# Optimization experiments

Hardware: AMD Instinct MI355X
Metric: run time of the kernel (lower is better)

Reference implementation:

```python
import jax, jax.numpy as jnp
import numpy as np

N, E = 50000, 800000
DIN, DH, DOUT = 128, 128, 64


def setup_inputs() -> dict:
    key = jax.random.key(0)
    k = jax.random.split(key, 6)
    node_features = jax.random.normal(k[0], (N, DIN), dtype=jnp.float32)
    edge_src = jax.random.randint(k[1], (E,), 0, N)
    edge_dst = jax.random.randint(k[2], (E,), 0, N)
    # Glorot-ish init for the two GCNConv weight matrices, zero bias (PyG default bias=True)
    W1 = jax.random.normal(k[3], (DIN, DH), dtype=jnp.float32) * (1.0 / np.sqrt(DIN))
    b1 = jnp.zeros((DH,), dtype=jnp.float32)
    W2 = jax.random.normal(k[4], (DH, DOUT), dtype=jnp.float32) * (1.0 / np.sqrt(DH))
    b2 = jnp.zeros((DOUT,), dtype=jnp.float32)
    return {"node_features": node_features, "edge_src": edge_src, "edge_dst": edge_dst,
            "W1": W1, "b1": b1, "W2": W2, "b2": b2}


def gcn_conv(x, W, b, src, dst, n):
    """PyG GCNConv: add self-loops, symmetric D^-1/2 (A+I) D^-1/2 normalization."""
    xw = x @ W  # [n, d_out]
    loops = jnp.arange(n, dtype=src.dtype)
    s = jnp.concatenate([src, loops])  # edges + self-loops
    d = jnp.concatenate([dst, loops])
    deg = jax.ops.segment_sum(jnp.ones_like(d, dtype=xw.dtype), d, num_segments=n)
    dinv = jnp.where(deg > 0, jax.lax.rsqrt(deg), 0.0)
    norm = dinv[s] * dinv[d]  # [E + n]
    msg = xw[s] * norm[:, None]  # gather + scale (memory-bound)
    out = jax.ops.segment_sum(msg, d, num_segments=n)  # scatter-add
    return out + b


def reference(node_features, edge_src, edge_dst, W1, b1, W2, b2):
    n = node_features.shape[0]
    h = gcn_conv(node_features, W1, b1, edge_src, edge_dst, n)
    h = jax.nn.relu(h)  # dropout omitted (inference / eval mode)
    h = gcn_conv(h, W2, b2, edge_src, edge_dst, n)
    # EdgePredictor: per-edge dot product of endpoint representations
    score = jnp.sum(h[edge_src] * h[edge_dst], axis=-1)  # [E]
    return score
```

## Files before the change

### kernel.cpp

```cpp
#include <hip/hip_runtime.h>
#include <hip/hip_bf16.h>
#include <type_traits>


#define DIN 128
#define DH  128
#define DOUT 64
#define BSH 7
#define BNODES 128
#define CAP 2560
#define QSH 13
#define POISON 0xAAAAAAAAu

typedef __attribute__((ext_vector_type(8))) short short8;
typedef __attribute__((ext_vector_type(4))) float floatx4;

__device__ inline float2 bf2_to_f2(unsigned u) {
    union { unsigned i; float f; } a, b;
    a.i = u << 16;
    b.i = u & 0xffff0000u;
    return make_float2(a.f, b.f);
}
__device__ inline float bf_to_f(unsigned short u) {
    union { unsigned i; float f; } a;
    a.i = ((unsigned)u) << 16;
    return a.f;
}
__device__ inline unsigned short f_to_bf(float f) {
    union { float f; unsigned i; } v; v.f = f;
    unsigned r = v.i + 0x7fffu + ((v.i >> 16) & 1u);
    return (unsigned short)(r >> 16);
}

__global__ __launch_bounds__(256) void place_gemm1_kernel(
    const int* __restrict__ src, const int* __restrict__ dst,
    unsigned* __restrict__ cursor, uint2* __restrict__ tmp, int E, int EB,
    const float* __restrict__ X, const float* __restrict__ W1,
    unsigned short* __restrict__ Y, int nrows) {
    __shared__ __align__(16) char smem[69632];
    int bid = blockIdx.x, t = threadIdx.x;

    if (bid < EB) {
        int* hist = (int*)smem;
        int* cur  = hist + 512;
        hist[t] = 0; hist[t + 256] = 0;
        __syncthreads();
        int base = bid * 4096 + t;
        int d[16];
#pragma unroll
        for (int it = 0; it < 16; ++it) {
            int e = base + it * 256;
            d[it] = (e < E) ? dst[e] : -1;
            if (d[it] >= 0) atomicAdd(&hist[d[it] >> BSH], 1);
        }
        __syncthreads();
#pragma unroll
        for (int k = t; k < 512; k += 256)
            if (hist[k])
                cur[k] = (int)(atomicAdd(&cursor[k], (unsigned)hist[k]) - POISON);
        __syncthreads();
#pragma unroll
        for (int it = 0; it < 16; ++it) {
            int e = base + it * 256;
            if (d[it] >= 0) {
                int bkt = d[it] >> BSH;
                int r = atomicAdd(&cur[bkt], 1);
                if (r >= 0 && r < CAP)
                    tmp[(size_t)bkt * CAP + r] =
                        make_uint2((unsigned)src[e] |
                                   ((unsigned)(d[it] & (BNODES - 1)) << 16),
                                   (unsigned)e);
            }
        }
        return;
    }

    constexpr int KP = 136;
    unsigned short* Xs = (unsigned short*)smem;
    unsigned short* Wt = Xs + 128 * KP;
    int row0 = (bid - EB) * 128;

#pragma unroll
    for (int it = 0; it < 16; ++it) {
        int idx = it * 256 + t;
        int r = idx >> 5;
        int c4 = (idx & 31) * 4;
        int gr = row0 + r; if (gr >= nrows) gr = nrows - 1;
        float4 v = *(const float4*)(X + (size_t)gr * 128 + c4);
        ushort4 p;
        p.x = f_to_bf(v.x); p.y = f_to_bf(v.y);
        p.z = f_to_bf(v.z); p.w = f_to_bf(v.w);
        *(ushort4*)&Xs[r * KP + c4] = p;
    }
#pragma unroll
    for (int it = 0; it < 16; ++it) {
        int idx = it * 256 + t;
        int n = idx >> 5;
        int k4 = (idx & 31) * 4;
        ushort4 p;
        p.x = f_to_bf(W1[(size_t)(k4 + 0) * 128 + n]);
        p.y = f_to_bf(W1[(size_t)(k4 + 1) * 128 + n]);
        p.z = f_to_bf(W1[(size_t)(k4 + 2) * 128 + n]);
        p.w = f_to_bf(W1[(size_t)(k4 + 3) * 128 + n]);
        *(ushort4*)&Wt[n * KP + k4] = p;
    }
    __syncthreads();

    int wv = t >> 6, lane = t & 63;
    int lr = lane & 15;
    int lk = (lane >> 4) * 8;
    int rw = wv * 32;

    floatx4 acc[2][8];
#pragma unroll
    for (int rt = 0; rt < 2; ++rt)
#pragma unroll
        for (int ct = 0; ct < 8; ++ct) acc[rt][ct] = (floatx4){0.f, 0.f, 0.f, 0.f};

#pragma unroll
    for (int kk = 0; kk < 128; kk += 32) {
        short8 a[2], b[8];
#pragma unroll
        for (int rt = 0; rt < 2; ++rt)
            a[rt] = *(const short8*)&Xs[(rw + rt * 16 + lr) * KP + kk + lk];
#pragma unroll
        for (int ct = 0; ct < 8; ++ct)
            b[ct] = *(const short8*)&Wt[(ct * 16 + lr) * KP + kk + lk];
#pragma unroll
        for (int rt = 0; rt < 2; ++rt)
#pragma unroll
            for (int ct = 0; ct < 8; ++ct)
                acc[rt][ct] = __builtin_amdgcn_mfma_f32_16x16x32_bf16(
                    a[rt], b[ct], acc[rt][ct], 0, 0, 0);
    }
#pragma unroll
    for (int rt = 0; rt < 2; ++rt) {
#pragma unroll
        for (int i = 0; i < 4; ++i) {
            int grow = row0 + rw + rt * 16 + (lane >> 4) * 4 + i;
            if (grow >= nrows) continue;
#pragma unroll
            for (int ct = 0; ct < 8; ++ct)
                Y[(size_t)grow * 128 + ct * 16 + lr] = f_to_bf(acc[rt][ct][i]);
        }
    }
}

__global__ __launch_bounds__(512) void bucket_csr_kernel(const uint2* __restrict__ tmp,
                                                         const unsigned* __restrict__ cursor,
                                                         int* __restrict__ row_beg,
                                                         int* __restrict__ row_end,
                                                         float* __restrict__ dinv,
                                                         int* __restrict__ col,
                                                         int* __restrict__ eidx, int N) {
    __shared__ int hist[1024], cur[1024];
    __shared__ int wsum[8];
    __shared__ unsigned ebuf[CAP];
    __shared__ unsigned ibuf[CAP];
    __shared__ unsigned ssrc[CAP];
    __shared__ unsigned sidx[CAP];
    int b = blockIdx.x, t = threadIdx.x;
    int lane = t & 63, wv = t >> 6;
    int size = (int)(cursor[b] - POISON);
    if (size < 0) size = 0;
    if (size > CAP) size = CAP;
    size_t rbase = (size_t)b * CAP;
    hist[t] = 0; hist[t + 512] = 0;
    __syncthreads();
    for (int i = t; i < size; i += 512) {
        uint2 e = tmp[rbase + i];
        ebuf[i] = e.x;
        ibuf[i] = e.y;
        int key = (int)(e.x >> 16) * 8 + (int)((e.x & 0xffffu) >> QSH);
        atomicAdd(&hist[key], 1);
    }
    __syncthreads();
    int l0 = hist[t * 2], l1 = hist[t * 2 + 1];
    int s = l0 + l1;
    int run = s;
#pragma unroll
    for (int off = 1; off < 64; off <<= 1) {
        int u = __shfl_up(run, off);
        if (lane >= off) run += u;
    }
    if (lane == 63) wsum[wv] = run;
    __syncthreads();
    int woff = 0;
#pragma unroll
    for (int k = 0; k < 8; ++k) woff += (k < wv) ? wsum[k] : 0;
    int excl = woff + run - s;
    hist[t * 2] = excl;       cur[t * 2] = excl;
    hist[t * 2 + 1] = excl + l0; cur[t * 2 + 1] = excl + l0;
    __syncthreads();
    if (t < BNODES) {
        int node = b * BNODES + t;
        if (node < N) {
            int nbeg = hist[t * 8];
            int nend = (t == BNODES - 1) ? size : hist[t * 8 + 8];
            row_beg[node] = (int)rbase + nbeg;
            row_end[node] = (int)rbase + nend;
            dinv[node] = rsqrtf((float)(nend - nbeg + 1));
        }
    }
    __syncthreads();
    for (int i = t; i < size; i += 512) {
        unsigned e = ebuf[i];
        int key = (int)(e >> 16) * 8 + (int)((e & 0xffffu) >> QSH);
        int r = atomicAdd(&cur[key], 1);
        ssrc[r] = e & 0xffffu;
        sidx[r] = ibuf[i];
    }
    __syncthreads();
    for (int i = t; i < size; i += 512) {
        col[rbase + i]  = (int)ssrc[i];
        eidx[rbase + i] = (int)sidx[i];
    }
}

__global__ __launch_bounds__(256) void agg1_kernel(const unsigned short* __restrict__ y1,
                                                   const int* __restrict__ row_beg,
                                                   const int* __restrict__ row_end,
                                                   const int* __restrict__ col,
                                                   const float* __restrict__ dinv,
                                                   const float* __restrict__ b1,
                                                   unsigned short* __restrict__ h1, int n) {
    int w = (blockIdx.x * 256 + threadIdx.x) >> 6;
    int lane = threadIdx.x & 63;
    if (w >= n) return;
    float dw = dinv[w];
    float acc0, acc1;
    {
        float2 t2 = bf2_to_f2(*(const unsigned*)(y1 + (size_t)w * 128 + lane * 2));
        acc0 = dw * t2.x; acc1 = dw * t2.y;
    }
    int beg = row_beg[w], end = row_end[w];
    int i = beg;
    for (; i + 8 <= end; i += 8) {
        int s[8];
#pragma unroll
        for (int u = 0; u < 8; ++u) s[u] = col[i + u];
        float dv[8];
#pragma unroll
        for (int u = 0; u < 8; ++u) dv[u] = dinv[s[u]];
        unsigned tv[8];
#pragma unroll
        for (int u = 0; u < 8; ++u)
            tv[u] = *(const unsigned*)(y1 + (size_t)s[u] * 128 + lane * 2);
#pragma unroll
        for (int u = 0; u < 8; ++u) {
            float2 f = bf2_to_f2(tv[u]);
            acc0 = fmaf(dv[u], f.x, acc0);
            acc1 = fmaf(dv[u], f.y, acc1);
        }
    }
    for (; i < end; ++i) {
        int s = col[i];
        float dv = dinv[s];
        float2 f = bf2_to_f2(*(const unsigned*)(y1 + (size_t)s * 128 + lane * 2));
        acc0 = fmaf(dv, f.x, acc0);
        acc1 = fmaf(dv, f.y, acc1);
    }
    float r0 = fmaxf(fmaf(dw, acc0, b1[lane * 2]), 0.f);
    float r1 = fmaxf(fmaf(dw, acc1, b1[lane * 2 + 1]), 0.f);
    unsigned pk = (unsigned)f_to_bf(r0) | ((unsigned)f_to_bf(r1) << 16);
    *(unsigned*)(h1 + (size_t)w * 128 + lane * 2) = pk;
}

__global__ __launch_bounds__(256) void mfma_gemm2_kernel(const unsigned short* __restrict__ X,
                                                         const float* __restrict__ W,
                                                         const float* __restrict__ dinv,
                                                         unsigned short* __restrict__ Y,
                                                         int nrows) {
    constexpr int KP = 136;
    __shared__ unsigned short Xs[128 * KP];
    __shared__ unsigned short Wt[64 * KP];
    int tid = threadIdx.x;
    int row0 = blockIdx.x * 128;

#pragma unroll
    for (int it = 0; it < 8; ++it) {
        int idx = it * 256 + tid;
        int r = idx >> 4;
        int c8 = (idx & 15) * 8;
        int gr = row0 + r; if (gr >= nrows) gr = nrows - 1;
        uint4 v = *(const uint4*)(X + (size_t)gr * 128 + c8);
        *(uint4*)&Xs[r * KP + c8] = v;
    }
#pragma unroll
    for (int it = 0; it < 8; ++it) {
        int idx = it * 256 + tid;
        int n = idx >> 5;
        int k4 = (idx & 31) * 4;
        ushort4 p;
        p.x = f_to_bf(W[(size_t)(k4 + 0) * 64 + n]);
        p.y = f_to_bf(W[(size_t)(k4 + 1) * 64 + n]);
        p.z = f_to_bf(W[(size_t)(k4 + 2) * 64 + n]);
        p.w = f_to_bf(W[(size_t)(k4 + 3) * 64 + n]);
        *(ushort4*)&Wt[n * KP + k4] = p;
    }
    __syncthreads();

    int wv = tid >> 6, lane = tid & 63;
    int lr = lane & 15;
    int lk = (lane >> 4) * 8;
    int rw = wv * 32;

    floatx4 acc[2][4];
#pragma unroll
    for (int rt = 0; rt < 2; ++rt)
#pragma unroll
        for (int ct = 0; ct < 4; ++ct) acc[rt][ct] = (floatx4){0.f, 0.f, 0.f, 0.f};

#pragma unroll
    for (int kk = 0; kk < 128; kk += 32) {
        short8 a[2], b[4];
#pragma unroll
        for (int rt = 0; rt < 2; ++rt)
            a[rt] = *(const short8*)&Xs[(rw + rt * 16 + lr) * KP + kk + lk];
#pragma unroll
        for (int ct = 0; ct < 4; ++ct)
            b[ct] = *(const short8*)&Wt[(ct * 16 + lr) * KP + kk + lk];
#pragma unroll
        for (int rt = 0; rt < 2; ++rt)
#pragma unroll
            for (int ct = 0; ct < 4; ++ct)
                acc[rt][ct] = __builtin_amdgcn_mfma_f32_16x16x32_bf16(
                    a[rt], b[ct], acc[rt][ct], 0, 0, 0);
    }
#pragma unroll
    for (int rt = 0; rt < 2; ++rt) {
#pragma unroll
        for (int i = 0; i < 4; ++i) {
            int grow = row0 + rw + rt * 16 + (lane >> 4) * 4 + i;
            if (grow >= nrows) continue;
            float dv = dinv[grow];
#pragma unroll
            for (int ct = 0; ct < 4; ++ct)
                Y[(size_t)grow * 64 + ct * 16 + lr] = f_to_bf(acc[rt][ct][i] * dv);
        }
    }
}

__global__ __launch_bounds__(256) void agg2_kernel(const unsigned short* __restrict__ y,
                                                   const int* __restrict__ row_beg,
                                                   const int* __restrict__ row_end,
                                                   const int* __restrict__ col,
                                                   const float* __restrict__ dinv,
                                                   const float* __restrict__ bias,
                                                   unsigned short* __restrict__ out, int n) {
    int w = (blockIdx.x * 256 + threadIdx.x) >> 6;
    int lane = threadIdx.x & 63;
    if (w >= n) return;
    float acc = bf_to_f(y[(size_t)w * 64 + lane]);
    int beg = row_beg[w], end = row_end[w];
    int i = beg;
    for (; i + 8 <= end; i += 8) {
        int s[8];
#pragma unroll
        for (int u = 0; u < 8; ++u) s[u] = col[i + u];
        unsigned short tv[8];
#pragma unroll
        for (int u = 0; u < 8; ++u) tv[u] = y[(size_t)s[u] * 64 + lane];
#pragma unroll
        for (int u = 0; u < 8; ++u) acc += bf_to_f(tv[u]);
    }
    for (; i < end; ++i) acc += bf_to_f(y[(size_t)col[i] * 64 + lane]);
    float r = fmaf(dinv[w], acc, bias[lane]);
    out[(size_t)w * 64 + lane] = f_to_bf(r);
}

__global__ __launch_bounds__(256) void score_csr_kernel(const unsigned short* __restrict__ h2,
                                                        const int* __restrict__ row_beg,
                                                        const int* __restrict__ row_end,
                                                        const int* __restrict__ col,
                                                        const int* __restrict__ eidx,
                                                        float* __restrict__ out, int n) {
    int w = (blockIdx.x * 256 + threadIdx.x) >> 6;
    int lane = threadIdx.x & 63;
    if (w >= n) return;
    int q = lane & 7;
    uint4 hd = *(const uint4*)(h2 + (size_t)w * 64 + q * 8);
    float d0[8];
    { float2 f;
      f = bf2_to_f2(hd.x); d0[0] = f.x; d0[1] = f.y;
      f = bf2_to_f2(hd.y); d0[2] = f.x; d0[3] = f.y;
      f = bf2_to_f2(hd.z); d0[4] = f.x; d0[5] = f.y;
      f = bf2_to_f2(hd.w); d0[6] = f.x; d0[7] = f.y; }
    int beg = row_beg[w], end = row_end[w];
    int g = lane >> 3;
    for (int i = beg; i < end; i += 8) {
        int ei = i + g;
        bool ok = ei < end;
        int s = ok ? col[ei] : 0;
        uint4 hs = *(const uint4*)(h2 + (size_t)s * 64 + q * 8);
        float v = 0.f;
        float2 f;
        f = bf2_to_f2(hs.x); v = fmaf(d0[0], f.x, v); v = fmaf(d0[1], f.y, v);
        f = bf2_to_f2(hs.y); v = fmaf(d0[2], f.x, v); v = fmaf(d0[3], f.y, v);
        f = bf2_to_f2(hs.z); v = fmaf(d0[4], f.x, v); v = fmaf(d0[5], f.y, v);
        f = bf2_to_f2(hs.w); v = fmaf(d0[6], f.x, v); v = fmaf(d0[7], f.y, v);
        v += __shfl_xor(v, 4);
        v += __shfl_xor(v, 2);
        v += __shfl_xor(v, 1);
        if (ok && q == 0) out[eidx[ei]] = v;
    }
}

extern "C" void kernel_launch(void* const* d_in, const int* in_sizes, int n_in,
                              void* d_out, int out_size, void* d_ws, size_t ws_size,
                              hipStream_t stream) {
    const float* X   = (const float*)d_in[0];
    const int*   src = (const int*)d_in[1];
    const int*   dst = (const int*)d_in[2];
    const float* W1  = (const float*)d_in[3];
    const float* b1  = (const float*)d_in[4];
    const float* W2  = (const float*)d_in[5];
    const float* b2  = (const float*)d_in[6];
    float* score = (float*)d_out;

    const int N = in_sizes[0] / DIN;
    const int E = in_sizes[1];
    const int nbuck = (N + BNODES - 1) / BNODES;
    const int EB = (E + 4095) / 4096;
    const int GB = (N + 127) / 128;

    auto align = [](size_t x) { return (x + 255) & ~(size_t)255; };
    char* p = (char*)d_ws;
    unsigned* cursor = (unsigned*)p;        p += align(512 * 4);
    int*   row_beg = (int*)p;               p += align((size_t)N * 4);
    int*   row_end = (int*)p;               p += align((size_t)N * 4);
    float* dinv    = (float*)p;             p += align((size_t)N * 4);
    int*   col     = (int*)p;               p += align((size_t)nbuck * CAP * 4);
    int*   eidx    = (int*)p;               p += align((size_t)nbuck * CAP * 4);
    uint2* tmp     = (uint2*)p;             p += align((size_t)nbuck * CAP * 8);
    unsigned short* y1 = (unsigned short*)p; p += align((size_t)N * DH * 2);
    unsigned short* h1 = (unsigned short*)p; p += align((size_t)N * DH * 2);
    unsigned short* y2 = y1;
    unsigned short* h2 = y1 + (size_t)N * DOUT;

    place_gemm1_kernel<<<EB + GB, 256, 0, stream>>>(src, dst, cursor, tmp, E, EB,
                                                    X, W1, y1, N);
    bucket_csr_kernel<<<nbuck, 512, 0, stream>>>(tmp, cursor, row_beg, row_end,
                                                 dinv, col, eidx, N);

    int agg_blocks = (N + 3) / 4;
    agg1_kernel<<<agg_blocks, 256, 0, stream>>>(y1, row_beg, row_end, col,
                                                dinv, b1, h1, N);

    mfma_gemm2_kernel<<<GB, 256, 0, stream>>>(h1, W2, dinv, y2, N);

    agg2_kernel<<<agg_blocks, 256, 0, stream>>>(y2, row_beg, row_end, col,
                                                dinv, b2, h2, N);
    score_csr_kernel<<<agg_blocks, 256, 0, stream>>>(h2, row_beg, row_end,
                                                     col, eidx, score, N);
}
```

Before: 232.0 us.

## Widen gather loads in aggregation kernels and unroll score loop over two edges

Both aggregation kernels now split each wavefront into four 16-lane groups. Each group gathers a different neighbor row with 16-byte (agg1) or 8-byte (agg2) vector loads, so one load instruction covers four edges instead of one. Partial sums are combined across groups with xor shuffles, and only the first group writes the output. The score kernel processes two edge batches per iteration for more loads in flight, and all three kernels get an occupancy hint in launch bounds. In exchange there is extra shuffle work, more registers per thread, and some wasted lanes on tail iterations for low-degree nodes.

```diff
diff --git a/kernel.cpp b/kernel.cpp
--- a/kernel.cpp
+++ b/kernel.cpp
@@ -217,53 +217,84 @@
     }
 }
 
-__global__ __launch_bounds__(256) void agg1_kernel(const unsigned short* __restrict__ y1,
-                                                   const int* __restrict__ row_beg,
-                                                   const int* __restrict__ row_end,
-                                                   const int* __restrict__ col,
-                                                   const float* __restrict__ dinv,
-                                                   const float* __restrict__ b1,
-                                                   unsigned short* __restrict__ h1, int n) {
+__global__ __launch_bounds__(256, 8) void agg1_kernel(const unsigned short* __restrict__ y1,
+                                                      const int* __restrict__ row_beg,
+                                                      const int* __restrict__ row_end,
+                                                      const int* __restrict__ col,
+                                                      const float* __restrict__ dinv,
+                                                      const float* __restrict__ b1,
+                                                      unsigned short* __restrict__ h1, int n) {
     int w = (blockIdx.x * 256 + threadIdx.x) >> 6;
     int lane = threadIdx.x & 63;
     if (w >= n) return;
+    int q = lane & 15;
+    int g = lane >> 4;
     float dw = dinv[w];
-    float acc0, acc1;
+    float acc[8];
     {
-        float2 t2 = bf2_to_f2(*(const unsigned*)(y1 + (size_t)w * 128 + lane * 2));
-        acc0 = dw * t2.x; acc1 = dw * t2.y;
+        uint4 hv = *(const uint4*)(y1 + (size_t)w * 128 + q * 8);
+        float selfw = (g == 0) ? dw : 0.f;
+        float2 f;
+        f = bf2_to_f2(hv.x); acc[0] = selfw * f.x; acc[1] = selfw * f.y;
+        f = bf2_to_f2(hv.y); acc[2] = selfw * f.x; acc[3] = selfw * f.y;
+        f = bf2_to_f2(hv.z); acc[4] = selfw * f.x; acc[5] = selfw * f.y;
+        f = bf2_to_f2(hv.w); acc[6] = selfw * f.x; acc[7] = selfw * f.y;
     }
     int beg = row_beg[w], end = row_end[w];
     int i = beg;
-    for (; i + 8 <= end; i += 8) {
-        int s[8];
-#pragma unroll
-        for (int u = 0; u < 8; ++u) s[u] = col[i + u];
-        float dv[8];
-#pragma unroll
-        for (int u = 0; u < 8; ++u) dv[u] = dinv[s[u]];
-        unsigned tv[8];
-#pragma unroll
-        for (int u = 0; u < 8; ++u)
-            tv[u] = *(const unsigned*)(y1 + (size_t)s[u] * 128 + lane * 2);
-#pragma unroll
-        for (int u = 0; u < 8; ++u) {
-            float2 f = bf2_to_f2(tv[u]);
-            acc0 = fmaf(dv[u], f.x, acc0);
-            acc1 = fmaf(dv[u], f.y, acc1);
-        }
-    }
-    for (; i < end; ++i) {
-        int s = col[i];
-        float dv = dinv[s];
-        float2 f = bf2_to_f2(*(const unsigned*)(y1 + (size_t)s * 128 + lane * 2));
-        acc0 = fmaf(dv, f.x, acc0);
-        acc1 = fmaf(dv, f.y, acc1);
-    }
-    float r0 = fmaxf(fmaf(dw, acc0, b1[lane * 2]), 0.f);
-    float r1 = fmaxf(fmaf(dw, acc1, b1[lane * 2 + 1]), 0.f);
-    unsigned pk = (unsigned)f_to_bf(r0) | ((unsigned)f_to_bf(r1) << 16);
-    *(unsigned*)(h1 + (size_t)w * 128 + lane * 2) = pk;
+    for (; i + 16 <= end; i += 16) {
+        int s4[4];
+#pragma unroll
+        for (int u = 0; u < 4; ++u) s4[u] = col[i + u * 4 + g];
+        float dv[4];
+#pragma unroll
+        for (int u = 0; u < 4; ++u) dv[u] = dinv[s4[u]];
+        uint4 tv[4];
+#pragma unroll
+        for (int u = 0; u < 4; ++u)
+            tv[u] = *(const uint4*)(y1 + (size_t)s4[u] * 128 + q * 8);
+#pragma unroll
+        for (int u = 0; u < 4; ++u) {
+            float2 f;
+            f = bf2_to_f2(tv[u].x); acc[0] = fmaf(dv[u], f.x, acc[0]); acc[1] = fmaf(dv[u], f.y, acc[1]);
+            f = bf2_to_f2(tv[u].y); acc[2] = fmaf(dv[u], f.x, acc[2]); acc[3] = fmaf(dv[u], f.y, acc[3]);
+            f = bf2_to_f2(tv[u].z); acc[4] = fmaf(dv[u], f.x, acc[4]); acc[5] = fmaf(dv[u], f.y, acc[5]);
+            f = bf2_to_f2(tv[u].w); acc[6] = fmaf(dv[u], f.x, acc[6]); acc[7] = fmaf(dv[u], f.y, acc[7]);
+        }
+    }
+    for (; i < end; i += 4) {
+        int r = i + g;
+        bool ok = r < end;
+        int sv = ok ? col[r] : col[i];
+        float dv = ok ? dinv[sv] : 0.f;
+        uint4 tv = *(const uint4*)(y1 + (size_t)sv * 128 + q * 8);
+        float2 f;
+        f = bf2_to_f2(tv.x); acc[0] = fmaf(dv, f.x, acc[0]); acc[1] = fmaf(dv, f.y, acc[1]);
+        f = bf2_to_f2(tv.y); acc[2] = fmaf(dv, f.x, acc[2]); acc[3] = fmaf(dv, f.y, acc[3]);
+        f = bf2_to_f2(tv.z); acc[4] = fmaf(dv, f.x, acc[4]); acc[5] = fmaf(dv, f.y, acc[5]);
+        f = bf2_to_f2(tv.w); acc[6] = fmaf(dv, f.x, acc[6]); acc[7] = fmaf(dv, f.y, acc[7]);
+    }
+#pragma unroll
+    for (int j = 0; j < 8; ++j) {
+        acc[j] += __shfl_xor(acc[j], 16);
+        acc[j] += __shfl_xor(acc[j], 32);
+    }
+    if (g == 0) {
+        float r0 = fmaxf(fmaf(dw, acc[0], b1[q * 8 + 0]), 0.f);
+        float r1 = fmaxf(fmaf(dw, acc[1], b1[q * 8 + 1]), 0.f);
+        float r2 = fmaxf(fmaf(dw, acc[2], b1[q * 8 + 2]), 0.f);
+        float r3 = fmaxf(fmaf(dw, acc[3], b1[q * 8 + 3]), 0.f);
+        float r4 = fmaxf(fmaf(dw, acc[4], b1[q * 8 + 4]), 0.f);
+        float r5 = fmaxf(fmaf(dw, acc[5], b1[q * 8 + 5]), 0.f);
+        float r6 = fmaxf(fmaf(dw, acc[6], b1[q * 8 + 6]), 0.f);
+        float r7 = fmaxf(fmaf(dw, acc[7], b1[q * 8 + 7]), 0.f);
+        uint4 pk;
+        pk.x = (unsigned)f_to_bf(r0) | ((unsigned)f_to_bf(r1) << 16);
+        pk.y = (unsigned)f_to_bf(r2) | ((unsigned)f_to_bf(r3) << 16);
+        pk.z = (unsigned)f_to_bf(r4) | ((unsigned)f_to_bf(r5) << 16);
+        pk.w = (unsigned)f_to_bf(r6) | ((unsigned)f_to_bf(r7) << 16);
+        *(uint4*)(h1 + (size_t)w * 128 + q * 8) = pk;
+    }
 }
 
 __global__ __launch_bounds__(256) void mfma_gemm2_kernel(const unsigned short* __restrict__ X,
@@ -341,40 +372,77 @@
     }
 }
 
-__global__ __launch_bounds__(256) void agg2_kernel(const unsigned short* __restrict__ y,
-                                                   const int* __restrict__ row_beg,
-                                                   const int* __restrict__ row_end,
-                                                   const int* __restrict__ col,
-                                                   const float* __restrict__ dinv,
-                                                   const float* __restrict__ bias,
-                                                   unsigned short* __restrict__ out, int n) {
+__global__ __launch_bounds__(256, 8) void agg2_kernel(const unsigned short* __restrict__ y,
+                                                      const int* __restrict__ row_beg,
+                                                      const int* __restrict__ row_end,
+                                                      const int* __restrict__ col,
+                                                      const float* __restrict__ dinv,
+                                                      const float* __restrict__ bias,
+                                                      unsigned short* __restrict__ out, int n) {
     int w = (blockIdx.x * 256 + threadIdx.x) >> 6;
     int lane = threadIdx.x & 63;
     if (w >= n) return;
-    float acc = bf_to_f(y[(size_t)w * 64 + lane]);
+    int q = lane & 15;
+    int g = lane >> 4;
+    float acc[4];
+    {
+        uint2 sv = *(const uint2*)(y + (size_t)w * 64 + q * 4);
+        float selfw = (g == 0) ? 1.f : 0.f;
+        float2 f;
+        f = bf2_to_f2(sv.x); acc[0] = selfw * f.x; acc[1] = selfw * f.y;
+        f = bf2_to_f2(sv.y); acc[2] = selfw * f.x; acc[3] = selfw * f.y;
+    }
     int beg = row_beg[w], end = row_end[w];
     int i = beg;
-    for (; i + 8 <= end; i += 8) {
-        int s[8];
-#pragma unroll
-        for (int u = 0; u < 8; ++u) s[u] = col[i + u];
-        unsigned short tv[8];
-#pragma unroll
-        for (int u = 0; u < 8; ++u) tv[u] = y[(size_t)s[u] * 64 + lane];
-#pragma unroll
-        for (int u = 0; u < 8; ++u) acc += bf_to_f(tv[u]);
-    }
-    for (; i < end; ++i) acc += bf_to_f(y[(size_t)col[i] * 64 + lane]);
-    float r = fmaf(dinv[w], acc, bias[lane]);
-    out[(size_t)w * 64 + lane] = f_to_bf(r);
-}
-
-__global__ __launch_bounds__(256) void score_csr_kernel(const unsigned short* __restrict__ h2,
-                                                        const int* __restrict__ row_beg,
-                                                        const int* __restrict__ row_end,
-                                                        const int* __restrict__ col,
-                                                        const int* __restrict__ eidx,
-                                                        float* __restrict__ out, int n) {
+    for (; i + 32 <= end; i += 32) {
+        int s8[8];
+#pragma unroll
+        for (int u = 0; u < 8; ++u) s8[u] = col[i + u * 4 + g];
+        uint2 tv[8];
+#pragma unroll
+        for (int u = 0; u < 8; ++u)
+            tv[u] = *(const uint2*)(y + (size_t)s8[u] * 64 + q * 4);
+#pragma unroll
+        for (int u = 0; u < 8; ++u) {
+            float2 f;
+            f = bf2_to_f2(tv[u].x); acc[0] += f.x; acc[1] += f.y;
+            f = bf2_to_f2(tv[u].y); acc[2] += f.x; acc[3] += f.y;
+        }
+    }
+    for (; i < end; i += 4) {
+        int r = i + g;
+        bool ok = r < end;
+        int sv = ok ? col[r] : col[i];
+        float m = ok ? 1.f : 0.f;
+        uint2 tv = *(const uint2*)(y + (size_t)sv * 64 + q * 4);
+        float2 f;
+        f = bf2_to_f2(tv.x); acc[0] = fmaf(m, f.x, acc[0]); acc[1] = fmaf(m, f.y, acc[1]);
+        f = bf2_to_f2(tv.y); acc[2] = fmaf(m, f.x, acc[2]); acc[3] = fmaf(m, f.y, acc[3]);
+    }
+#pragma unroll
+    for (int j = 0; j < 4; ++j) {
+        acc[j] += __shfl_xor(acc[j], 16);
+        acc[j] += __shfl_xor(acc[j], 32);
+    }
+    if (g == 0) {
+        float dw = dinv[w];
+        float r0 = fmaf(dw, acc[0], bias[q * 4 + 0]);
+        float r1 = fmaf(dw, acc[1], bias[q * 4 + 1]);
+        float r2 = fmaf(dw, acc[2], bias[q * 4 + 2]);
+        float r3 = fmaf(dw, acc[3], bias[q * 4 + 3]);
+        uint2 pk;
+        pk.x = (unsigned)f_to_bf(r0) | ((unsigned)f_to_bf(r1) << 16);
+        pk.y = (unsigned)f_to_bf(r2) | ((unsigned)f_to_bf(r3) << 16);
+        *(uint2*)(out + (size_t)w * 64 + q * 4) = pk;
+    }
+}
+
+__global__ __launch_bounds__(256, 8) void score_csr_kernel(const unsigned short* __restrict__ h2,
+                                                           const int* __restrict__ row_beg,
+                                                           const int* __restrict__ row_end,
+                                                           const int* __restrict__ col,
+                                                           const int* __restrict__ eidx,
+                                                           float* __restrict__ out, int n) {
     int w = (blockIdx.x * 256 + threadIdx.x) >> 6;
     int lane = threadIdx.x & 63;
     if (w >= n) return;
@@ -388,21 +456,31 @@
       f = bf2_to_f2(hd.w); d0[6] = f.x; d0[7] = f.y; }
     int beg = row_beg[w], end = row_end[w];
     int g = lane >> 3;
-    for (int i = beg; i < end; i += 8) {
-        int ei = i + g;
-        bool ok = ei < end;
-        int s = ok ? col[ei] : 0;
-        uint4 hs = *(const uint4*)(h2 + (size_t)s * 64 + q * 8);
-        float v = 0.f;
+    for (int i = beg; i < end; i += 16) {
+        int ei0 = i + g, ei1 = i + 8 + g;
+        bool ok0 = ei0 < end, ok1 = ei1 < end;
+        int s0 = ok0 ? col[ei0] : col[i];
+        int s1 = ok1 ? col[ei1] : col[i];
+        uint4 hs0 = *(const uint4*)(h2 + (size_t)s0 * 64 + q * 8);
+        uint4 hs1 = *(const uint4*)(h2 + (size_t)s1 * 64 + q * 8);
+        float v0 = 0.f, v1 = 0.f;
         float2 f;
-        f = bf2_to_f2(hs.x); v = fmaf(d0[0], f.x, v); v = fmaf(d0[1], f.y, v);
-        f = bf2_to_f2(hs.y); v = fmaf(d0[2], f.x, v); v = fmaf(d0[3], f.y, v);
-        f = bf2_to_f2(hs.z); v = fmaf(d0[4], f.x, v); v = fmaf(d0[5], f.y, v);
-        f = bf2_to_f2(hs.w); v = fmaf(d0[6], f.x, v); v = fmaf(d0[7], f.y, v);
-        v += __shfl_xor(v, 4);
-        v += __shfl_xor(v, 2);
-        v += __shfl_xor(v, 1);
-        if (ok && q == 0) out[eidx[ei]] = v;
+        f = bf2_to_f2(hs0.x); v0 = fmaf(d0[0], f.x, v0); v0 = fmaf(d0[1], f.y, v0);
+        f = bf2_to_f2(hs0.y); v0 = fmaf(d0[2], f.x, v0); v0 = fmaf(d0[3], f.y, v0);
+        f = bf2_to_f2(hs0.z); v0 = fmaf(d0[4], f.x, v0); v0 = fmaf(d0[5], f.y, v0);
+        f = bf2_to_f2(hs0.w); v0 = fmaf(d0[6], f.x, v0); v0 = fmaf(d0[7], f.y, v0);
+        f = bf2_to_f2(hs1.x); v1 = fmaf(d0[0], f.x, v1); v1 = fmaf(d0[1], f.y, v1);
+        f = bf2_to_f2(hs1.y); v1 = fmaf(d0[2], f.x, v1); v1 = fmaf(d0[3], f.y, v1);
+        f = bf2_to_f2(hs1.z); v1 = fmaf(d0[4], f.x, v1); v1 = fmaf(d0[5], f.y, v1);
+        f = bf2_to_f2(hs1.w); v1 = fmaf(d0[6], f.x, v1); v1 = fmaf(d0[7], f.y, v1);
+        v0 += __shfl_xor(v0, 4);
+        v0 += __shfl_xor(v0, 2);
+        v0 += __shfl_xor(v0, 1);
+        v1 += __shfl_xor(v1, 4);
+        v1 += __shfl_xor(v1, 2);
+        v1 += __shfl_xor(v1, 1);
+        if (ok0 && q == 0) out[eidx[ei0]] = v0;
+        if (ok1 && q == 0) out[eidx[ei1]] = v1;
     }
 }
 
```

Measured after the change: 222.5 us. -4.1%, faster.
